# Kernel tuning notes

Hardware: AMD Instinct MI355X
Metric: run time of the kernel (lower is better)

Reference implementation:

```python
import jax, jax.numpy as jnp
import numpy as np

NUM_ATOM_TYPE = 120
NUM_BOND_TYPE = 6
NUM_LAYER = 5
EMB_DIM = 300
N_NODES = 50000
N_EDGES = 800000
BN_EPS = 1e-5


def setup_inputs() -> dict:
    key = jax.random.key(0)
    ks = jax.random.split(key, 12)
    x = jax.random.randint(ks[0], (N_NODES, 2), 0, NUM_ATOM_TYPE, dtype=jnp.int32)
    edge_index = jax.random.randint(ks[1], (2, N_EDGES), 0, N_NODES, dtype=jnp.int32)
    edge_attr = jax.random.randint(ks[2], (N_EDGES, 2), 0, 3, dtype=jnp.int32)
    s = 1.0 / np.sqrt(EMB_DIM)
    x_emb = jax.random.uniform(ks[3], (NUM_ATOM_TYPE, EMB_DIM), minval=-s, maxval=s, dtype=jnp.float32)
    edge_emb = jax.random.uniform(ks[4], (NUM_LAYER, NUM_BOND_TYPE, EMB_DIM), minval=-s, maxval=s, dtype=jnp.float32)
    W1 = jax.random.normal(ks[5], (NUM_LAYER, EMB_DIM, 2 * EMB_DIM), dtype=jnp.float32) * s
    b1 = jnp.zeros((NUM_LAYER, 2 * EMB_DIM), dtype=jnp.float32)
    W2 = jax.random.normal(ks[6], (NUM_LAYER, 2 * EMB_DIM, EMB_DIM), dtype=jnp.float32) * (1.0 / np.sqrt(2 * EMB_DIM))
    b2 = jnp.zeros((NUM_LAYER, EMB_DIM), dtype=jnp.float32)
    bn_gamma = jnp.ones((NUM_LAYER, EMB_DIM), dtype=jnp.float32)
    bn_beta = jnp.zeros((NUM_LAYER, EMB_DIM), dtype=jnp.float32)
    return {"x": x, "edge_index": edge_index, "edge_attr": edge_attr,
            "x_emb": x_emb, "edge_emb": edge_emb,
            "W1": W1, "b1": b1, "W2": W2, "b2": b2,
            "bn_gamma": bn_gamma, "bn_beta": bn_beta}


def _forward(x, edge_index, edge_attr, x_emb, edge_emb, W1, b1, W2, b2, bn_gamma, bn_beta):
    n = x.shape[0]
    # node embedding: sum of x_embedding1 over feature columns (faithful to source)
    h = x_emb[x[:, 0]] + x_emb[x[:, 1]]  # [N, D]
    # add self loops once (same for every layer)
    loop = jnp.arange(n, dtype=edge_index.dtype)
    src = jnp.concatenate([edge_index[0], loop])  # [E+N]
    dst = jnp.concatenate([edge_index[1], loop])
    # self-loop edge_attr: zeros with column 0 = 4
    sl = jnp.zeros((n, edge_attr.shape[1]), dtype=edge_attr.dtype).at[:, 0].set(4)
    ea = jnp.concatenate([edge_attr, sl], axis=0)  # [E+N, 2]
    for layer in range(NUM_LAYER):
        # edge embeddings: sum of edge_embedding1 over attr columns (faithful)
        ee = edge_emb[layer][ea[:, 0]] + edge_emb[layer][ea[:, 1]]  # [E+N, D]
        msg = h[src] + ee
        agg = jax.ops.segment_sum(msg, dst, num_segments=n)  # scatter-add
        # GIN MLP (classification branch applies mlp to aggregate only)
        hid = jax.nn.relu(agg @ W1[layer] + b1[layer])
        h = hid @ W2[layer] + b2[layer]
        # BatchNorm1d, training-mode batch statistics
        mu = jnp.mean(h, axis=0)
        var = jnp.var(h, axis=0)
        h = (h - mu) * jax.lax.rsqrt(var + BN_EPS) * bn_gamma[layer] + bn_beta[layer]
        if layer != NUM_LAYER - 1:
            h = jax.nn.relu(h)
        # dropout ratio is 0 -> no-op
    return h  # JK == 'last'


def reference(x, edge_index, edge_attr, x_emb, edge_emb, W1, b1, W2, b2, bn_gamma, bn_beta):
    return _forward(x, edge_index, edge_attr, x_emb, edge_emb, W1, b1, W2, b2, bn_gamma, bn_beta)
```

## Files before the change

### kernel.cpp

```cpp
#include <hip/hip_runtime.h>
#include <hip/hip_bf16.h>

typedef unsigned short u16;
typedef _Float16 f16;
typedef f16 f16x8 __attribute__((ext_vector_type(8)));
typedef u16 u16x8 __attribute__((ext_vector_type(8)));
typedef float f32x4 __attribute__((ext_vector_type(4)));

#define NN 50000
#define NE 800000
#define D  300
#define DP 320
#define HP 640

__device__ __forceinline__ float h2f(u16 u){ f16 h = __builtin_bit_cast(f16, u); return (float)h; }
__device__ __forceinline__ u16 f2h(float f){ f16 h = (f16)f; return __builtin_bit_cast(u16, h); }

__device__ __forceinline__ void gl_lds16(const void* g, void* l){
  __builtin_amdgcn_global_load_lds((const __attribute__((address_space(1))) unsigned int*)g,
                                   (__attribute__((address_space(3))) unsigned int*)l, 16, 0, 0);
}

__device__ __forceinline__ f32x4 mfma_f16(u16x8 a, u16x8 b, f32x4 c){
  return __builtin_amdgcn_mfma_f32_16x16x32_f16(__builtin_bit_cast(f16x8, a),
                                                __builtin_bit_cast(f16x8, b), c, 0, 0, 0);
}

__global__ void k_count(const int* __restrict__ ei, int* __restrict__ cnt){
  int e = blockIdx.x * 256 + threadIdx.x;
  if (e < NE) atomicAdd(&cnt[ei[NE + e]], 1);
}

__global__ void k_scan1(const int* __restrict__ cnt, int* __restrict__ rp, int* __restrict__ bsum){
  __shared__ int s[1024];
  int i = blockIdx.x * 1024 + threadIdx.x;
  int v = (i < NN) ? cnt[i] : 0;
  s[threadIdx.x] = v;
  __syncthreads();
  for (int off = 1; off < 1024; off <<= 1){
    int t = (threadIdx.x >= off) ? s[threadIdx.x - off] : 0;
    __syncthreads();
    s[threadIdx.x] += t;
    __syncthreads();
  }
  if (i < NN) rp[i] = s[threadIdx.x] - v;
  if (threadIdx.x == 1023) bsum[blockIdx.x] = s[1023];
}

__global__ void k_scan2(int* __restrict__ bsum, int nb){
  __shared__ int s[64];
  int v = (threadIdx.x < nb) ? bsum[threadIdx.x] : 0;
  s[threadIdx.x] = v; __syncthreads();
  for (int off = 1; off < 64; off <<= 1){
    int t = (threadIdx.x >= off) ? s[threadIdx.x - off] : 0;
    __syncthreads();
    s[threadIdx.x] += t;
    __syncthreads();
  }
  if (threadIdx.x < nb) bsum[threadIdx.x] = s[threadIdx.x] - v;
}

__global__ void k_scan3(int* __restrict__ rp, int* __restrict__ cur, const int* __restrict__ bsum){
  int i = blockIdx.x * 256 + threadIdx.x;
  if (i < NN){ int v = rp[i] + bsum[i >> 10]; rp[i] = v; cur[i] = v; }
  if (i == 0) rp[NN] = NE;
}

__global__ void k_fill(const int* __restrict__ ei, const int* __restrict__ ea,
                       int* __restrict__ cur, int* __restrict__ pack){
  int e = blockIdx.x * 256 + threadIdx.x;
  if (e >= NE) return;
  int d = ei[NE + e];
  int pos = atomicAdd(&cur[d], 1);
  pack[pos] = ei[e] | ((ea[2*e] * 3 + ea[2*e + 1]) << 16);
}

__global__ void k_wconv(const float* __restrict__ W1, const float* __restrict__ W2,
                        u16* __restrict__ W1t, u16* __restrict__ W2t){
  int i = blockIdx.x * 256 + threadIdx.x;
  {
    int l = i / (HP * DP); int rem = i % (HP * DP); int n = rem / DP, k = rem % DP;
    float v = (n < 600 && k < D) ? W1[((size_t)l * D + k) * 600 + n] : 0.f;
    W1t[i] = f2h(v);
  }
  {
    int l = i / (DP * HP); int rem = i % (DP * HP); int n = rem / HP, k = rem % HP;
    float v = (n < D && k < 600) ? W2[((size_t)l * 600 + k) * D + n] : 0.f;
    W2t[i] = f2h(v);
  }
}

__global__ void k_nodeemb(const int* __restrict__ x, const float* __restrict__ xemb, u16* __restrict__ hb){
  int v = blockIdx.x, c = threadIdx.x;
  float y = 0.f;
  if (c < D){
    int a = x[2*v], b = x[2*v + 1];
    y = xemb[(size_t)a * D + c] + xemb[(size_t)b * D + c];
  }
  hb[(size_t)v * DP + c] = f2h(y);
}

__global__ __launch_bounds__(256) void k_agg(const u16* __restrict__ hb, const int* __restrict__ rp,
    const int* __restrict__ pack, const float* __restrict__ eemb, u16* __restrict__ agg){
  __shared__ float ec[10 * DP];
  for (int i = threadIdx.x; i < 10 * DP; i += 256){
    int t = i / DP, c = i % DP;
    float v = 0.f;
    if (c < D){
      int a0 = (t == 9) ? 4 : (t / 3), a1 = (t == 9) ? 0 : (t % 3);
      v = eemb[a0 * D + c] + eemb[a1 * D + c];
    }
    ec[i] = v;
  }
  __syncthreads();
  int wid = threadIdx.x >> 6, lane = threadIdx.x & 63;
  int v = blockIdx.x * 4 + wid;
  if (v >= NN) return;
  float acc[5];
  const u16* hv = hb + (size_t)v * DP;
  #pragma unroll
  for (int j = 0; j < 5; ++j){
    int c = lane + 64 * j;
    acc[j] = h2f(hv[c]) + ec[9 * DP + c];
  }
  int p = rp[v], p1 = rp[v + 1];
  for (; p + 2 <= p1; p += 2){
    int pk0 = pack[p], pk1 = pack[p + 1];
    const u16* h0 = hb + (size_t)(pk0 & 0xFFFF) * DP;
    const u16* h1 = hb + (size_t)(pk1 & 0xFFFF) * DP;
    const float* e0 = &ec[(pk0 >> 16) * DP];
    const float* e1 = &ec[(pk1 >> 16) * DP];
    u16 t0[5], t1[5];
    #pragma unroll
    for (int j = 0; j < 5; ++j){ int c = lane + 64 * j; t0[j] = h0[c]; t1[j] = h1[c]; }
    #pragma unroll
    for (int j = 0; j < 5; ++j){
      int c = lane + 64 * j;
      acc[j] += (h2f(t0[j]) + e0[c]) + (h2f(t1[j]) + e1[c]);
    }
  }
  if (p < p1){
    int pk0 = pack[p];
    const u16* h0 = hb + (size_t)(pk0 & 0xFFFF) * DP;
    const float* e0 = &ec[(pk0 >> 16) * DP];
    #pragma unroll
    for (int j = 0; j < 5; ++j){
      int c = lane + 64 * j;
      acc[j] += h2f(h0[c]) + e0[c];
    }
  }
  #pragma unroll
  for (int j = 0; j < 5; ++j) agg[(size_t)v * DP + lane + 64 * j] = f2h(acc[j]);
}

template<int KPAD, bool RELU, int OUTM>
__global__ __launch_bounds__(256) void k_gemm(const u16* __restrict__ A, const u16* __restrict__ Bt,
    const float* __restrict__ bias, int bias_n,
    void* __restrict__ C, int ldc, int ccols, int M, int Nrows){
  __shared__ __attribute__((aligned(16))) u16 lA[128 * 32];
  __shared__ __attribute__((aligned(16))) u16 lB[128 * 32];
  const int tid = threadIdx.x;
  const int lane = tid & 63;
  const int wid = tid >> 6;
  const int gm0 = blockIdx.x * 128, gn0 = blockIdx.y * 128;
  const int wr = (wid >> 1) * 64, wc = (wid & 1) * 64;
  int ar1 = gm0 + (tid >> 2);       if (ar1 >= M) ar1 = M - 1;
  int ar2 = gm0 + 64 + (tid >> 2);  if (ar2 >= M) ar2 = M - 1;
  int br1 = gn0 + (tid >> 2);       if (br1 >= Nrows) br1 = Nrows - 1;
  int br2 = gn0 + 64 + (tid >> 2);  if (br2 >= Nrows) br2 = Nrows - 1;
  const int kb = (tid & 3) * 8;
  const int wbase = (tid & ~63) * 8;
  f32x4 acc[4][4] = {};
  for (int k0 = 0; k0 < KPAD; k0 += 32){
    __syncthreads();
    gl_lds16(A  + (size_t)ar1 * KPAD + k0 + kb, lA + wbase);
    gl_lds16(A  + (size_t)ar2 * KPAD + k0 + kb, lA + wbase + 2048);
    gl_lds16(Bt + (size_t)br1 * KPAD + k0 + kb, lB + wbase);
    gl_lds16(Bt + (size_t)br2 * KPAD + k0 + kb, lB + wbase + 2048);
    asm volatile("s_waitcnt vmcnt(0)" ::: "memory");
    __syncthreads();
    u16x8 af[4], bfr[4];
    #pragma unroll
    for (int m = 0; m < 4; ++m) af[m]  = *(const u16x8*)&lA[(wr + m * 16 + (lane & 15)) * 32 + (lane >> 4) * 8];
    #pragma unroll
    for (int n = 0; n < 4; ++n) bfr[n] = *(const u16x8*)&lB[(wc + n * 16 + (lane & 15)) * 32 + (lane >> 4) * 8];
    #pragma unroll
    for (int m = 0; m < 4; ++m)
      #pragma unroll
      for (int n = 0; n < 4; ++n)
        acc[m][n] = mfma_f16(af[m], bfr[n], acc[m][n]);
  }
  #pragma unroll
  for (int m = 0; m < 4; ++m){
    const int row0 = gm0 + wr + m * 16 + (lane >> 4) * 4;
    #pragma unroll
    for (int n = 0; n < 4; ++n){
      const int col = gn0 + wc + n * 16 + (lane & 15);
      if (col >= ccols) continue;
      const float bv = (col < bias_n) ? bias[col] : 0.f;
      #pragma unroll
      for (int r = 0; r < 4; ++r){
        const int row = row0 + r;
        if (row < M){
          float vv = acc[m][n][r] + bv;
          if (RELU) vv = fmaxf(vv, 0.f);
          if (OUTM == 0) ((float*)C)[(size_t)row * ldc + col] = vv;
          else           ((u16*)C)[(size_t)row * ldc + col] = f2h(vv);
        }
      }
    }
  }
}

__global__ void k_bnstats(const float* __restrict__ h2, float* __restrict__ sums){
  int c = threadIdx.x;
  if (c >= D) return;
  int r0 = blockIdx.x * 250, r1 = r0 + 250;
  float s = 0.f, q = 0.f;
  for (int r = r0; r < r1; ++r){
    float v = h2[(size_t)r * D + c];
    s += v; q += v * v;
  }
  atomicAdd(&sums[c], s);
  atomicAdd(&sums[DP + c], q);
}

template<bool LAST>
__global__ void k_bnapply(const float* h2, const float* __restrict__ sums,
    const float* __restrict__ gamma, const float* __restrict__ beta,
    u16* __restrict__ hb, float* outp){
  int r = blockIdx.x, c = threadIdx.x;
  float y = 0.f;
  if (c < D){
    float mu  = sums[c] * (1.f / NN);
    float var = sums[DP + c] * (1.f / NN) - mu * mu;
    float x = h2[(size_t)r * D + c];
    float s = var + 1e-5f;
    float inv = rsqrtf(s);
    inv = inv * (1.5f - 0.5f * s * inv * inv);
    y = (x - mu) * inv * gamma[c] + beta[c];
    if (!LAST) y = fmaxf(y, 0.f);
  }
  if (LAST){ if (c < D) outp[(size_t)r * D + c] = y; }
  else hb[(size_t)r * DP + c] = f2h(y);
}

extern "C" void kernel_launch(void* const* d_in, const int* in_sizes, int n_in,
                              void* d_out, int out_size, void* d_ws, size_t ws_size,
                              hipStream_t stream){
  (void)in_sizes; (void)n_in; (void)out_size; (void)ws_size;
  const int*   x    = (const int*)d_in[0];
  const int*   ei   = (const int*)d_in[1];
  const int*   ea   = (const int*)d_in[2];
  const float* xemb = (const float*)d_in[3];
  const float* eemb = (const float*)d_in[4];
  const float* W1   = (const float*)d_in[5];
  const float* b1   = (const float*)d_in[6];
  const float* W2   = (const float*)d_in[7];
  const float* b2   = (const float*)d_in[8];
  const float* gam  = (const float*)d_in[9];
  const float* bet  = (const float*)d_in[10];
  float* out = (float*)d_out;

  char* w = (char*)d_ws;
  size_t off = 0;
  auto alloc = [&](size_t b){ void* p = w + off; off += (b + 255) & ~(size_t)255; return p; };
  u16* hid   = (u16*)alloc((size_t)NN * HP * 2);
  u16* hb    = hid;
  u16* aggb  = (u16*)alloc((size_t)NN * DP * 2);
  u16* W1t   = (u16*)alloc((size_t)5 * HP * DP * 2);
  u16* W2t   = (u16*)alloc((size_t)5 * DP * HP * 2);
  int* rp    = (int*)alloc((NN + 1) * 4);
  int* cnt   = (int*)alloc((size_t)NN * 4);
  int* cur   = (int*)alloc((size_t)NN * 4);
  int* bsum  = (int*)alloc(64 * 4);
  int* pack  = (int*)alloc((size_t)NE * 4);
  float* sums= (float*)alloc(2 * DP * 4);
  float* h2  = out;

  hipMemsetAsync(cnt, 0, NN * 4, stream);
  k_count<<<NE / 256, 256, 0, stream>>>(ei, cnt);
  k_scan1<<<(NN + 1023) / 1024, 1024, 0, stream>>>(cnt, rp, bsum);
  k_scan2<<<1, 64, 0, stream>>>(bsum, (NN + 1023) / 1024);
  k_scan3<<<(NN + 255) / 256, 256, 0, stream>>>(rp, cur, bsum);
  k_fill<<<NE / 256, 256, 0, stream>>>(ei, ea, cur, pack);
  k_wconv<<<(5 * HP * DP) / 256, 256, 0, stream>>>(W1, W2, W1t, W2t);
  k_nodeemb<<<NN, DP, 0, stream>>>(x, xemb, hb);

  for (int l = 0; l < 5; ++l){
    k_agg<<<(NN + 3) / 4, 256, 0, stream>>>(hb, rp, pack, eemb + (size_t)l * 6 * D, aggb);
    k_gemm<DP, true, 1><<<dim3((NN + 127) / 128, HP / 128), 256, 0, stream>>>(
        aggb, W1t + (size_t)l * HP * DP, b1 + l * 600, 600, hid, HP, HP, NN, HP);
    k_gemm<HP, false, 0><<<dim3((NN + 127) / 128, 3), 256, 0, stream>>>(
        hid, W2t + (size_t)l * DP * HP, b2 + l * D, D, h2, D, D, NN, DP);
    hipMemsetAsync(sums, 0, 2 * DP * 4, stream);
    k_bnstats<<<200, DP, 0, stream>>>(h2, sums);
    if (l < 4) k_bnapply<false><<<NN, DP, 0, stream>>>(h2, sums, gam + l * D, bet + l * D, hb, nullptr);
    else       k_bnapply<true ><<<NN, DP, 0, stream>>>(h2, sums, gam + l * D, bet + l * D, nullptr, out);
  }
}
```

Measured before the change: 1.541 ms.

## Factor edge embeddings into per-node type counts, vectorize aggregation, fuse BN stats into GEMM

The aggregation kernel no longer adds an edge embedding per edge. It counts bond-type combinations per destination node once during setup and applies the edge-embedding contribution as a weighted sum of the four embedding rows, which removes per-edge LDS reads and adds. Neighbour feature loads become wider, packed half2 loads: 8 bytes plus 4 bytes per lane instead of five scalar u16 loads. BatchNorm sum and sum-of-squares are now accumulated in the second GEMM's epilogue with shuffles and atomics, replacing the separate stats kernel and its full re-read of h2. This adds a per-node count buffer and an extra atomic pass at setup, and float atomics make the summation order nondeterministic.

Measured after the change: 1.536 ms. Within noise of the previous version (-0.3%).

```diff
diff --git a/kernel.cpp b/kernel.cpp
--- a/kernel.cpp
+++ b/kernel.cpp
@@ -4,6 +4,7 @@
 typedef unsigned short u16;
 typedef _Float16 f16;
 typedef f16 f16x8 __attribute__((ext_vector_type(8)));
+typedef f16 half2t __attribute__((ext_vector_type(2)));
 typedef u16 u16x8 __attribute__((ext_vector_type(8)));
 typedef float f32x4 __attribute__((ext_vector_type(4)));
 
@@ -15,6 +16,9 @@
 
 __device__ __forceinline__ float h2f(u16 u){ f16 h = __builtin_bit_cast(f16, u); return (float)h; }
 __device__ __forceinline__ u16 f2h(float f){ f16 h = (f16)f; return __builtin_bit_cast(u16, h); }
+__device__ __forceinline__ float hlo(unsigned u){ half2t h = __builtin_bit_cast(half2t, u); return (float)h.x; }
+__device__ __forceinline__ float hhi(unsigned u){ half2t h = __builtin_bit_cast(half2t, u); return (float)h.y; }
+__device__ __forceinline__ unsigned packh(float x, float y){ half2t h; h.x = (f16)x; h.y = (f16)y; return __builtin_bit_cast(unsigned, h); }
 
 __device__ __forceinline__ void gl_lds16(const void* g, void* l){
   __builtin_amdgcn_global_load_lds((const __attribute__((address_space(1))) unsigned int*)g,
@@ -26,9 +30,15 @@
                                                 __builtin_bit_cast(f16x8, b), c, 0, 0, 0);
 }
 
-__global__ void k_count(const int* __restrict__ ei, int* __restrict__ cnt){
+__global__ void k_count(const int* __restrict__ ei, const int* __restrict__ ea,
+                        int* __restrict__ cnt, int* __restrict__ ccnt){
   int e = blockIdx.x * 256 + threadIdx.x;
-  if (e < NE) atomicAdd(&cnt[ei[NE + e]], 1);
+  if (e < NE){
+    int d = ei[NE + e];
+    atomicAdd(&cnt[d], 1);
+    int t = ea[2*e] * 3 + ea[2*e + 1];
+    atomicAdd(&ccnt[d * 12 + t], 1);
+  }
 }
 
 __global__ void k_scan1(const int* __restrict__ cnt, int* __restrict__ rp, int* __restrict__ bsum){
@@ -66,13 +76,12 @@
   if (i == 0) rp[NN] = NE;
 }
 
-__global__ void k_fill(const int* __restrict__ ei, const int* __restrict__ ea,
-                       int* __restrict__ cur, int* __restrict__ pack){
+__global__ void k_fill(const int* __restrict__ ei, int* __restrict__ cur, int* __restrict__ pack){
   int e = blockIdx.x * 256 + threadIdx.x;
   if (e >= NE) return;
   int d = ei[NE + e];
   int pos = atomicAdd(&cur[d], 1);
-  pack[pos] = ei[e] | ((ea[2*e] * 3 + ea[2*e + 1]) << 16);
+  pack[pos] = ei[e];
 }
 
 __global__ void k_wconv(const float* __restrict__ W1, const float* __restrict__ W2,
@@ -101,62 +110,87 @@
 }
 
 __global__ __launch_bounds__(256) void k_agg(const u16* __restrict__ hb, const int* __restrict__ rp,
-    const int* __restrict__ pack, const float* __restrict__ eemb, u16* __restrict__ agg){
-  __shared__ float ec[10 * DP];
-  for (int i = threadIdx.x; i < 10 * DP; i += 256){
+    const int* __restrict__ pack, const int* __restrict__ ccnt,
+    const float* __restrict__ eemb, u16* __restrict__ agg){
+  __shared__ float se[4 * DP];
+  for (int i = threadIdx.x; i < 4 * DP; i += 256){
     int t = i / DP, c = i % DP;
-    float v = 0.f;
-    if (c < D){
-      int a0 = (t == 9) ? 4 : (t / 3), a1 = (t == 9) ? 0 : (t % 3);
-      v = eemb[a0 * D + c] + eemb[a1 * D + c];
+    int row = (t == 3) ? 4 : t;
+    se[i] = (c < D) ? eemb[row * D + c] : 0.f;
+  }
+  __syncthreads();
+  const int wid = threadIdx.x >> 6, lane = threadIdx.x & 63;
+  const int v = blockIdx.x * 4 + wid;
+  if (v >= NN) return;
+  const char* __restrict__ hbb = (const char*)hb;
+  const unsigned lo8 = (unsigned)lane * 8u;
+  const unsigned lo4 = 512u + (unsigned)lane * 4u;
+  float a0, a1, a2, a3, a4 = 0.f, a5 = 0.f;
+  {
+    unsigned off = (unsigned)v * 640u;
+    uint2 u = *(const uint2*)(hbb + off + lo8);
+    a0 = hlo(u.x); a1 = hhi(u.x); a2 = hlo(u.y); a3 = hhi(u.y);
+    if (lane < 32){ unsigned uw = *(const unsigned*)(hbb + off + lo4); a4 = hlo(uw); a5 = hhi(uw); }
+  }
+  int p = rp[v];
+  const int pe = rp[v + 1];
+  for (; p + 2 <= pe; p += 2){
+    unsigned off0 = (unsigned)pack[p] * 640u;
+    unsigned off1 = (unsigned)pack[p + 1] * 640u;
+    uint2 u0 = *(const uint2*)(hbb + off0 + lo8);
+    uint2 u1 = *(const uint2*)(hbb + off1 + lo8);
+    unsigned w0v = 0, w1v = 0;
+    if (lane < 32){
+      w0v = *(const unsigned*)(hbb + off0 + lo4);
+      w1v = *(const unsigned*)(hbb + off1 + lo4);
     }
-    ec[i] = v;
-  }
-  __syncthreads();
-  int wid = threadIdx.x >> 6, lane = threadIdx.x & 63;
-  int v = blockIdx.x * 4 + wid;
-  if (v >= NN) return;
-  float acc[5];
-  const u16* hv = hb + (size_t)v * DP;
-  #pragma unroll
-  for (int j = 0; j < 5; ++j){
-    int c = lane + 64 * j;
-    acc[j] = h2f(hv[c]) + ec[9 * DP + c];
-  }
-  int p = rp[v], p1 = rp[v + 1];
-  for (; p + 2 <= p1; p += 2){
-    int pk0 = pack[p], pk1 = pack[p + 1];
-    const u16* h0 = hb + (size_t)(pk0 & 0xFFFF) * DP;
-    const u16* h1 = hb + (size_t)(pk1 & 0xFFFF) * DP;
-    const float* e0 = &ec[(pk0 >> 16) * DP];
-    const float* e1 = &ec[(pk1 >> 16) * DP];
-    u16 t0[5], t1[5];
-    #pragma unroll
-    for (int j = 0; j < 5; ++j){ int c = lane + 64 * j; t0[j] = h0[c]; t1[j] = h1[c]; }
-    #pragma unroll
-    for (int j = 0; j < 5; ++j){
-      int c = lane + 64 * j;
-      acc[j] += (h2f(t0[j]) + e0[c]) + (h2f(t1[j]) + e1[c]);
-    }
-  }
-  if (p < p1){
-    int pk0 = pack[p];
-    const u16* h0 = hb + (size_t)(pk0 & 0xFFFF) * DP;
-    const float* e0 = &ec[(pk0 >> 16) * DP];
-    #pragma unroll
-    for (int j = 0; j < 5; ++j){
-      int c = lane + 64 * j;
-      acc[j] += h2f(h0[c]) + e0[c];
-    }
-  }
-  #pragma unroll
-  for (int j = 0; j < 5; ++j) agg[(size_t)v * DP + lane + 64 * j] = f2h(acc[j]);
+    a0 += hlo(u0.x) + hlo(u1.x);
+    a1 += hhi(u0.x) + hhi(u1.x);
+    a2 += hlo(u0.y) + hlo(u1.y);
+    a3 += hhi(u0.y) + hhi(u1.y);
+    a4 += hlo(w0v) + hlo(w1v);
+    a5 += hhi(w0v) + hhi(w1v);
+  }
+  if (p < pe){
+    unsigned off0 = (unsigned)pack[p] * 640u;
+    uint2 u0 = *(const uint2*)(hbb + off0 + lo8);
+    a0 += hlo(u0.x); a1 += hhi(u0.x); a2 += hlo(u0.y); a3 += hhi(u0.y);
+    if (lane < 32){ unsigned w0v = *(const unsigned*)(hbb + off0 + lo4); a4 += hlo(w0v); a5 += hhi(w0v); }
+  }
+  const int* cc = ccnt + (size_t)v * 12;
+  int4 cA = *(const int4*)cc;
+  int4 cB = *(const int4*)(cc + 4);
+  int c8 = cc[8];
+  float w0f = (float)(2 * cA.x + cA.y + cA.z + cA.w + cB.z + 1);
+  float w1f = (float)(cA.y + cA.w + 2 * cB.x + cB.y + cB.w);
+  float w2f = (float)(cA.z + cB.y + cB.z + cB.w + 2 * c8);
+  {
+    const float4 e0v = *(const float4*)&se[0 * DP + 4 * lane];
+    const float4 e1v = *(const float4*)&se[1 * DP + 4 * lane];
+    const float4 e2v = *(const float4*)&se[2 * DP + 4 * lane];
+    const float4 e4v = *(const float4*)&se[3 * DP + 4 * lane];
+    a0 += w0f * e0v.x + w1f * e1v.x + w2f * e2v.x + e4v.x;
+    a1 += w0f * e0v.y + w1f * e1v.y + w2f * e2v.y + e4v.y;
+    a2 += w0f * e0v.z + w1f * e1v.z + w2f * e2v.z + e4v.z;
+    a3 += w0f * e0v.w + w1f * e1v.w + w2f * e2v.w + e4v.w;
+  }
+  char* ab = (char*)agg;
+  unsigned oo = (unsigned)v * 640u;
+  uint2 st; st.x = packh(a0, a1); st.y = packh(a2, a3);
+  *(uint2*)(ab + oo + lo8) = st;
+  if (lane < 32){
+    int cI = 256 + 2 * lane;
+    a4 += w0f * se[0 * DP + cI]     + w1f * se[1 * DP + cI]     + w2f * se[2 * DP + cI]     + se[3 * DP + cI];
+    a5 += w0f * se[0 * DP + cI + 1] + w1f * se[1 * DP + cI + 1] + w2f * se[2 * DP + cI + 1] + se[3 * DP + cI + 1];
+    *(unsigned*)(ab + oo + lo4) = packh(a4, a5);
+  }
 }
 
 template<int KPAD, bool RELU, int OUTM>
 __global__ __launch_bounds__(256) void k_gemm(const u16* __restrict__ A, const u16* __restrict__ Bt,
     const float* __restrict__ bias, int bias_n,
-    void* __restrict__ C, int ldc, int ccols, int M, int Nrows){
+    void* __restrict__ C, int ldc, int ccols, int M, int Nrows,
+    float* __restrict__ sums){
   __shared__ __attribute__((aligned(16))) u16 lA[128 * 32];
   __shared__ __attribute__((aligned(16))) u16 lB[128 * 32];
   const int tid = threadIdx.x;
@@ -190,6 +224,7 @@
       for (int n = 0; n < 4; ++n)
         acc[m][n] = mfma_f16(af[m], bfr[n], acc[m][n]);
   }
+  float sn[4] = {0.f, 0.f, 0.f, 0.f}, qn[4] = {0.f, 0.f, 0.f, 0.f};
   #pragma unroll
   for (int m = 0; m < 4; ++m){
     const int row0 = gm0 + wr + m * 16 + (lane >> 4) * 4;
@@ -204,25 +239,29 @@
         if (row < M){
           float vv = acc[m][n][r] + bv;
           if (RELU) vv = fmaxf(vv, 0.f);
-          if (OUTM == 0) ((float*)C)[(size_t)row * ldc + col] = vv;
-          else           ((u16*)C)[(size_t)row * ldc + col] = f2h(vv);
+          if (OUTM == 0){
+            ((float*)C)[(size_t)row * ldc + col] = vv;
+            sn[n] += vv; qn[n] += vv * vv;
+          } else {
+            ((u16*)C)[(size_t)row * ldc + col] = f2h(vv);
+          }
         }
       }
     }
   }
-}
-
-__global__ void k_bnstats(const float* __restrict__ h2, float* __restrict__ sums){
-  int c = threadIdx.x;
-  if (c >= D) return;
-  int r0 = blockIdx.x * 250, r1 = r0 + 250;
-  float s = 0.f, q = 0.f;
-  for (int r = r0; r < r1; ++r){
-    float v = h2[(size_t)r * D + c];
-    s += v; q += v * v;
-  }
-  atomicAdd(&sums[c], s);
-  atomicAdd(&sums[DP + c], q);
+  if (OUTM == 0){
+    #pragma unroll
+    for (int n = 0; n < 4; ++n){
+      const int col = gn0 + wc + n * 16 + (lane & 15);
+      float s = sn[n], q = qn[n];
+      s += __shfl_xor(s, 16); q += __shfl_xor(q, 16);
+      s += __shfl_xor(s, 32); q += __shfl_xor(q, 32);
+      if (col < ccols && (lane >> 4) == 0){
+        atomicAdd(&sums[col], s);
+        atomicAdd(&sums[DP + col], q);
+      }
+    }
+  }
 }
 
 template<bool LAST>
@@ -275,26 +314,27 @@
   int* cur   = (int*)alloc((size_t)NN * 4);
   int* bsum  = (int*)alloc(64 * 4);
   int* pack  = (int*)alloc((size_t)NE * 4);
+  int* ccnt  = (int*)alloc((size_t)NN * 12 * 4);
   float* sums= (float*)alloc(2 * DP * 4);
   float* h2  = out;
 
   hipMemsetAsync(cnt, 0, NN * 4, stream);
-  k_count<<<NE / 256, 256, 0, stream>>>(ei, cnt);
+  hipMemsetAsync(ccnt, 0, (size_t)NN * 12 * 4, stream);
+  k_count<<<NE / 256, 256, 0, stream>>>(ei, ea, cnt, ccnt);
   k_scan1<<<(NN + 1023) / 1024, 1024, 0, stream>>>(cnt, rp, bsum);
   k_scan2<<<1, 64, 0, stream>>>(bsum, (NN + 1023) / 1024);
   k_scan3<<<(NN + 255) / 256, 256, 0, stream>>>(rp, cur, bsum);
-  k_fill<<<NE / 256, 256, 0, stream>>>(ei, ea, cur, pack);
+  k_fill<<<NE / 256, 256, 0, stream>>>(ei, cur, pack);
   k_wconv<<<(5 * HP * DP) / 256, 256, 0, stream>>>(W1, W2, W1t, W2t);
   k_nodeemb<<<NN, DP, 0, stream>>>(x, xemb, hb);
 
   for (int l = 0; l < 5; ++l){
-    k_agg<<<(NN + 3) / 4, 256, 0, stream>>>(hb, rp, pack, eemb + (size_t)l * 6 * D, aggb);
+    k_agg<<<(NN + 3) / 4, 256, 0, stream>>>(hb, rp, pack, ccnt, eemb + (size_t)l * 6 * D, aggb);
     k_gemm<DP, true, 1><<<dim3((NN + 127) / 128, HP / 128), 256, 0, stream>>>(
-        aggb, W1t + (size_t)l * HP * DP, b1 + l * 600, 600, hid, HP, HP, NN, HP);
+        aggb, W1t + (size_t)l * HP * DP, b1 + l * 600, 600, hid, HP, HP, NN, HP, nullptr);
+    hipMemsetAsync(sums, 0, 2 * DP * 4, stream);
     k_gemm<HP, false, 0><<<dim3((NN + 127) / 128, 3), 256, 0, stream>>>(
-        hid, W2t + (size_t)l * DP * HP, b2 + l * D, D, h2, D, D, NN, DP);
-    hipMemsetAsync(sums, 0, 2 * DP * 4, stream);
-    k_bnstats<<<200, DP, 0, stream>>>(h2, sums);
+        hid, W2t + (size_t)l * DP * HP, b2 + l * D, D, h2, D, D, NN, DP, sums);
     if (l < 4) k_bnapply<false><<<NN, DP, 0, stream>>>(h2, sums, gam + l * D, bet + l * D, hb, nullptr);
     else       k_bnapply<true ><<<NN, DP, 0, stream>>>(h2, sums, gam + l * D, bet + l * D, nullptr, out);
   }
```
